# Optimization experiments

Hardware: AMD Instinct MI355X
Metric: run time of the kernel (lower is better)

## Reference

```python
import jax, jax.numpy as jnp
import numpy as np

C = 4          # in_channels: number of TT objects in the input list
B = 4096       # batch_size
OUT = 32       # out_channels
ROWS = 17408   # in_channels * num_parameter = 4 * 4352


def setup_inputs() -> dict:
    key = jax.random.key(0)
    k1, k2, k3, k4 = jax.random.split(key, 4)
    cores_first = jax.random.normal(k1, (C, 128, B), dtype=jnp.float32)        # first core per TT object, flattened
    cores_mid = jax.random.normal(k2, (C, 2, 2048, B), dtype=jnp.float32)      # two middle cores per object
    cores_last = jax.random.normal(k3, (C, 128, B), dtype=jnp.float32)         # last core per object
    weight = jax.random.normal(k4, (ROWS, OUT), dtype=jnp.float32) * (1.0 / np.sqrt(ROWS))
    return {"cores_first": cores_first, "cores_mid": cores_mid,
            "cores_last": cores_last, "weight": weight}


def reference(cores_first, cores_mid, cores_last, weight):
    # Faithful to the torch loop: for each TT object, copy core0, core1, core2, core3
    # (each flattened to (-1, B)) into consecutive row blocks of buffer I, then GEMM.
    c, _, b = cores_first.shape
    # per-object row block in loop order: [first | mid0 | mid1 | last] -> (C, 4352, B)
    I = jnp.concatenate(
        [cores_first, cores_mid.reshape(c, -1, b), cores_last], axis=1
    ).reshape(-1, b)  # (ROWS, B)
    return jnp.einsum('io,ib->bo', weight, I)  # (B, OUT)
```

## Files before the change

### kernel.cpp

```cpp
#include <hip/hip_runtime.h>


#define BATCH  4096
#define OUTC   32
#define NCHUNK 34

__global__ __launch_bounds__(256) void cwl_partial(
    const float* __restrict__ cf,
    const float* __restrict__ cm,
    const float* __restrict__ cl,
    const float* __restrict__ w,
    float* __restrict__ ws)
{
    const int btile = blockIdx.x & 63;
    const int chunk = blockIdx.x >> 6;
    const int lane  = threadIdx.x & 63;
    const int wv    = threadIdx.x >> 6;
    const int o0    = __builtin_amdgcn_readfirstlane(wv * 8);
    const int b     = btile * 64 + lane;

    float acc[8];
#pragma unroll
    for (int k = 0; k < 8; ++k) acc[k] = 0.0f;

    for (int s = 0; s < 4; ++s) {
        const int m = chunk * 4 + s;
        const int c = m / 34;
        const int j = m - c * 34;
        const float* src;
        if (j == 0)
            src = cf + (size_t)c * 128 * BATCH;
        else if (j == 33)
            src = cl + (size_t)c * 128 * BATCH;
        else
            src = cm + ((size_t)c * 4096 + (size_t)(j - 1) * 128) * BATCH;

        const float* xp = src + b;
        const float* wp = w + (size_t)m * 128 * OUTC + o0;

#pragma unroll 8
        for (int r = 0; r < 128; ++r) {
            const float x = xp[(size_t)r * BATCH];
#pragma unroll
            for (int k = 0; k < 8; ++k)
                acc[k] = fmaf(x, wp[r * OUTC + k], acc[k]);
        }
    }

    float4* dst = (float4*)(ws + ((size_t)chunk * BATCH + b) * OUTC + o0);
    dst[0] = make_float4(acc[0], acc[1], acc[2], acc[3]);
    dst[1] = make_float4(acc[4], acc[5], acc[6], acc[7]);
}

__global__ __launch_bounds__(256) void cwl_reduce(
    const float* __restrict__ ws, float* __restrict__ out)
{
    const int idx = blockIdx.x * 256 + threadIdx.x;
    float s = 0.0f;
#pragma unroll
    for (int c = 0; c < NCHUNK; ++c)
        s += ws[(size_t)c * (BATCH * OUTC) + idx];
    out[idx] = s;
}

extern "C" void kernel_launch(void* const* d_in, const int* in_sizes, int n_in,
                              void* d_out, int out_size, void* d_ws, size_t ws_size,
                              hipStream_t stream)
{
    const float* cf = (const float*)d_in[0];
    const float* cm = (const float*)d_in[1];
    const float* cl = (const float*)d_in[2];
    const float* w  = (const float*)d_in[3];
    float* out = (float*)d_out;
    float* ws  = (float*)d_ws;

    cwl_partial<<<dim3(64 * NCHUNK), dim3(256), 0, stream>>>(cf, cm, cl, w, ws);
    cwl_reduce<<<dim3((BATCH * OUTC) / 256), dim3(256), 0, stream>>>(ws, out);
}
```

Before: 412.0 us.

## Stage weights in LDS and compute all 32 outputs per thread

Each thread now accumulates all 32 output channels for one batch column, so each input element is loaded once instead of once per wave in the block. Every 128x32 weight slice is staged into shared memory and read back as broadcast float4 values. Blocks now span 256 batch columns, cutting the grid from 2176 to 544 blocks. The cost is lower occupancy and fewer global loads in flight per CU, plus two barriers per slice, which could leave the streaming input reads latency-bound.

```diff
diff --git a/kernel.cpp b/kernel.cpp
--- a/kernel.cpp
+++ b/kernel.cpp
@@ -4,6 +4,7 @@
 #define BATCH  4096
 #define OUTC   32
 #define NCHUNK 34
+#define BTILES 16
 
 __global__ __launch_bounds__(256) void cwl_partial(
     const float* __restrict__ cf,
@@ -12,19 +13,19 @@
     const float* __restrict__ w,
     float* __restrict__ ws)
 {
-    const int btile = blockIdx.x & 63;
-    const int chunk = blockIdx.x >> 6;
-    const int lane  = threadIdx.x & 63;
-    const int wv    = threadIdx.x >> 6;
-    const int o0    = __builtin_amdgcn_readfirstlane(wv * 8);
-    const int b     = btile * 64 + lane;
+    __shared__ float wlds[128 * OUTC];
 
-    float acc[8];
+    const int chunk = blockIdx.x % NCHUNK;
+    const int btile = blockIdx.x / NCHUNK;
+    const int tid   = threadIdx.x;
+    const int b     = btile * 256 + tid;
+
+    float acc[OUTC];
 #pragma unroll
-    for (int k = 0; k < 8; ++k) acc[k] = 0.0f;
+    for (int j = 0; j < OUTC; ++j) acc[j] = 0.0f;
 
-    for (int s = 0; s < 4; ++s) {
-        const int m = chunk * 4 + s;
+    for (int h = 0; h < 4; ++h) {
+        const int m = chunk * 4 + h;
         const int c = m / 34;
         const int j = m - c * 34;
         const float* src;
@@ -35,32 +36,48 @@
         else
             src = cm + ((size_t)c * 4096 + (size_t)(j - 1) * 128) * BATCH;
 
-        const float* xp = src + b;
-        const float* wp = w + (size_t)m * 128 * OUTC + o0;
+        {
+            const float4* wg = (const float4*)(w + (size_t)m * 128 * OUTC);
+            float4* wl = (float4*)wlds;
+#pragma unroll
+            for (int k = 0; k < 4; ++k)
+                wl[tid + 256 * k] = wg[tid + 256 * k];
+        }
+        __syncthreads();
 
-#pragma unroll 8
+        const float*  xp  = src + b;
+        const float4* wl4 = (const float4*)wlds;
+#pragma unroll 4
         for (int r = 0; r < 128; ++r) {
             const float x = xp[(size_t)r * BATCH];
+            const float4* wr = wl4 + r * (OUTC / 4);
 #pragma unroll
-            for (int k = 0; k < 8; ++k)
-                acc[k] = fmaf(x, wp[r * OUTC + k], acc[k]);
+            for (int q = 0; q < OUTC / 4; ++q) {
+                const float4 wv = wr[q];
+                acc[4*q+0] = fmaf(x, wv.x, acc[4*q+0]);
+                acc[4*q+1] = fmaf(x, wv.y, acc[4*q+1]);
+                acc[4*q+2] = fmaf(x, wv.z, acc[4*q+2]);
+                acc[4*q+3] = fmaf(x, wv.w, acc[4*q+3]);
+            }
         }
+        __syncthreads();
     }
 
-    float4* dst = (float4*)(ws + ((size_t)chunk * BATCH + b) * OUTC + o0);
-    dst[0] = make_float4(acc[0], acc[1], acc[2], acc[3]);
-    dst[1] = make_float4(acc[4], acc[5], acc[6], acc[7]);
+    float4* dst = (float4*)(ws + ((size_t)chunk * BATCH + b) * OUTC);
+#pragma unroll
+    for (int q = 0; q < OUTC / 4; ++q)
+        dst[q] = make_float4(acc[4*q+0], acc[4*q+1], acc[4*q+2], acc[4*q+3]);
 }
 
 __global__ __launch_bounds__(256) void cwl_reduce(
     const float* __restrict__ ws, float* __restrict__ out)
 {
-    const int idx = blockIdx.x * 256 + threadIdx.x;
+    const int t = blockIdx.x * 256 + threadIdx.x;
     float s = 0.0f;
 #pragma unroll
     for (int c = 0; c < NCHUNK; ++c)
-        s += ws[(size_t)c * (BATCH * OUTC) + idx];
-    out[idx] = s;
+        s += ws[(size_t)c * (BATCH * OUTC) + t];
+    out[t] = s;
 }
 
 extern "C" void kernel_launch(void* const* d_in, const int* in_sizes, int n_in,
@@ -74,6 +91,6 @@
     float* out = (float*)d_out;
     float* ws  = (float*)d_ws;
 
-    cwl_partial<<<dim3(64 * NCHUNK), dim3(256), 0, stream>>>(cf, cm, cl, w, ws);
+    cwl_partial<<<dim3(NCHUNK * BTILES), dim3(256), 0, stream>>>(cf, cm, cl, w, ws);
     cwl_reduce<<<dim3((BATCH * OUTC) / 256), dim3(256), 0, stream>>>(ws, out);
 }
```

After: 501.0 us. 21.6% more time.
